# Kernel optimization log

Measured on AMD Instinct MI355X. Metric: run time of the kernel, lower is better.

## Reference

```python
import jax, jax.numpy as jnp
import numpy as np

B, S, Hd = 4, 2048, 1024
NH, D = 16, 64

def setup_inputs() -> dict:
    key = jax.random.key(0)
    ks = jax.random.split(key, 8)
    scale = 0.02
    return {
        "hidden_states": jax.random.normal(ks[0], (B, S, Hd), dtype=jnp.float32),
        "attention_mask": jnp.zeros((B, 1, 1, S), dtype=jnp.float32),
        "relations": jax.random.normal(ks[1], (1, 1, S, D), dtype=jnp.float32),
        "Wq": jax.random.normal(ks[2], (Hd, Hd), dtype=jnp.float32) * scale,
        "bq": jnp.zeros((Hd,), dtype=jnp.float32),
        "Wk": jax.random.normal(ks[3], (Hd, Hd), dtype=jnp.float32) * scale,
        "bk": jnp.zeros((Hd,), dtype=jnp.float32),
        "Wv": jax.random.normal(ks[4], (Hd, Hd), dtype=jnp.float32) * scale,
        "bv": jnp.zeros((Hd,), dtype=jnp.float32),
    }

def _heads(x):  # [B,S,Hd] -> [B,NH,S,D]
    return x.reshape(x.shape[0], x.shape[1], NH, D).transpose(0, 2, 1, 3)

def _rotate_half_interleaved(x):
    # stack([-x_odd, x_even], -1).reshape_as(x)
    return jnp.stack([-x[..., 1::2], x[..., ::2]], axis=-1).reshape(x.shape)

def reference(hidden_states, attention_mask, relations, Wq, bq, Wk, bk, Wv, bv):
    q = _heads(hidden_states @ Wq.T + bq)
    k = _heads(hidden_states @ Wk.T + bk)
    v = _heads(hidden_states @ Wv.T + bv)

    # interleaved rotary: cos from odd slots, sin from even slots, each repeated x2
    cos_pos = jnp.repeat(relations[..., 1::2], 2, axis=-1)  # [1,1,S,D]
    sin_pos = jnp.repeat(relations[..., ::2], 2, axis=-1)
    q = q * cos_pos + _rotate_half_interleaved(q) * sin_pos
    k = k * cos_pos + _rotate_half_interleaved(k) * sin_pos

    scores = jnp.einsum("bhqd,bhkd->bhqk", q, k) / jnp.sqrt(jnp.float32(D))
    scores = scores + attention_mask
    probs = jax.nn.softmax(scores, axis=-1)
    ctx = jnp.einsum("bhqk,bhkd->bhqd", probs, v)
    return ctx.transpose(0, 2, 1, 3).reshape(hidden_states.shape[0], hidden_states.shape[1], NH * D)
```

## Files before the change

### kernel.cpp

```cpp
#include <hip/hip_runtime.h>

typedef __attribute__((ext_vector_type(8))) short short8;
typedef __attribute__((ext_vector_type(4))) float f32x4;
typedef __attribute__((ext_vector_type(4))) unsigned int u32x4;
typedef __attribute__((ext_vector_type(2))) unsigned int u32x2;
typedef __attribute__((ext_vector_type(4))) unsigned short u16x4;

#define NHEADS 16
#define DHEAD 64
#define SEQ 2048
#define BATCH 4
#define HD 1024
#define MTOT 8192

static __device__ __forceinline__ unsigned short f2b(float x) {
  unsigned u = __builtin_bit_cast(unsigned, x);
  u += 0x7fffu + ((u >> 16) & 1u);
  return (unsigned short)(u >> 16);
}

static __device__ __forceinline__ unsigned pk2h(float lo, float hi) {
  unsigned a = __builtin_bit_cast(unsigned, lo) + 0x8000u;
  unsigned b = __builtin_bit_cast(unsigned, hi) + 0x8000u;
  return (a >> 16) | (b & 0xffff0000u);
}

static __device__ __forceinline__ void gll16(const void* g, void* l) {
  __builtin_amdgcn_global_load_lds(
      (const __attribute__((address_space(1))) unsigned int*)g,
      (__attribute__((address_space(3))) unsigned int*)l, 16, 0, 0);
}

__global__ void cvt_bf16(const float* __restrict__ src,
                         unsigned short* __restrict__ dst, int n4) {
  int i = blockIdx.x * blockDim.x + threadIdx.x;
  if (i < n4) {
    f32x4 v = ((const f32x4*)src)[i];
    u16x4 o;
    o[0] = f2b(v[0]); o[1] = f2b(v[1]); o[2] = f2b(v[2]); o[3] = f2b(v[3]);
    ((u16x4*)dst)[i] = o;
  }
}

#define WQ4 (HD * HD / 4)
__global__ void prep(const float* __restrict__ Wq, const float* __restrict__ Wk,
                     const float* __restrict__ Wv, const float* __restrict__ mask,
                     unsigned short* __restrict__ Wb,
                     unsigned short* __restrict__ Wm) {
  int i = blockIdx.x * blockDim.x + threadIdx.x;
  if (i < 3 * WQ4) {
    int rg = i / WQ4;
    int idx = i - rg * WQ4;
    const float* src = (rg == 0) ? Wq : (rg == 1) ? Wk : Wv;
    f32x4 v = ((const f32x4*)src)[idx];
    u16x4 o;
    o[0] = f2b(v[0]); o[1] = f2b(v[1]); o[2] = f2b(v[2]); o[3] = f2b(v[3]);
    ((u16x4*)(Wb + (size_t)rg * HD * HD))[idx] = o;
  } else {
    int j = i - 3 * WQ4;
    f32x4 v = ((const f32x4*)mask)[j];
    u16x4 o;
    o[0] = f2b(__expf(v[0])); o[1] = f2b(__expf(v[1]));
    o[2] = f2b(__expf(v[2])); o[3] = f2b(__expf(v[3]));
    ((u16x4*)Wm)[j] = o;
  }
}

__global__ __launch_bounds__(256) void qkv_gemm(
    const unsigned short* __restrict__ X,
    const unsigned short* __restrict__ Wall,
    const float* __restrict__ bq, const float* __restrict__ bk,
    const float* __restrict__ bv,
    const float* __restrict__ rel,
    const float* __restrict__ mask,
    unsigned short* __restrict__ Qo,
    unsigned short* __restrict__ Ko,
    unsigned short* __restrict__ Vt) {
  __shared__ __align__(16) unsigned short As[128 * 64];
  __shared__ __align__(16) unsigned short Bs[128 * 64];

  const int t = threadIdx.x;
  const int lane = t & 63;
  const int w = t >> 6;

  const int n = blockIdx.x;
  const int xcd = n & 7;
  const int li = n >> 3;
  const int pp = xcd * 3 + (li >> 6);
  const int bx = li & 63;
  const int by = pp & 7;
  const int bz = pp >> 3;

  const unsigned short* W = Wall + (size_t)bz * HD * HD;
  const int m0 = bx * 128;
  const int n0 = by * 128;

  f32x4 acc[4][4];
  for (int i = 0; i < 4; i++)
    for (int j = 0; j < 4; j++) acc[i][j] = (f32x4){0.f, 0.f, 0.f, 0.f};

  const int wm = (w & 1) * 64;
  const int wn = (w >> 1) * 64;
  const int cl = lane & 15;
  const int qd = lane >> 4;

  for (int k0 = 0; k0 < HD; k0 += 64) {
    __syncthreads();
#pragma unroll
    for (int j = 0; j < 4; j++) {
      int r0 = w * 32 + j * 8;
      int r = r0 + (lane >> 3);
      int cg = (((lane & 7) ^ (r & 7)) << 3);
      gll16(X + (size_t)(m0 + r) * HD + k0 + cg, As + r0 * 64);
      gll16(W + (size_t)(n0 + r) * HD + k0 + cg, Bs + r0 * 64);
    }
    __syncthreads();

#pragma unroll
    for (int ks = 0; ks < 2; ks++) {
      const int cc = ks * 4 + qd;
      short8 af[4], bf[4];
#pragma unroll
      for (int i = 0; i < 4; i++) {
        int r = wm + i * 16 + cl;
        af[i] = *(const short8*)(As + r * 64 + ((cc ^ (r & 7)) << 3));
      }
#pragma unroll
      for (int j = 0; j < 4; j++) {
        int r = wn + j * 16 + cl;
        bf[j] = *(const short8*)(Bs + r * 64 + ((cc ^ (r & 7)) << 3));
      }
      if (bz < 2) {
#pragma unroll
        for (int i = 0; i < 4; i++)
#pragma unroll
          for (int j = 0; j < 4; j++)
            acc[i][j] = __builtin_amdgcn_mfma_f32_16x16x32_bf16(bf[j], af[i],
                                                                acc[i][j], 0, 0, 0);
      } else {
#pragma unroll
        for (int i = 0; i < 4; i++)
#pragma unroll
          for (int j = 0; j < 4; j++)
            acc[i][j] = __builtin_amdgcn_mfma_f32_16x16x32_bf16(af[i], bf[j],
                                                                acc[i][j], 0, 0, 0);
      }
    }
  }

  if (bz == 2) {
    const int hh = (n0 + wn) >> 6;
#pragma unroll
    for (int i = 0; i < 4; i++) {
      int mb = m0 + wm + i * 16 + qd * 4;
      int bb = mb >> 11, ssb = mb & (SEQ - 1);
      f32x4 mk = *(const f32x4*)(mask + bb * SEQ + ssb);
      f32x4 w4;
#pragma unroll
      for (int r = 0; r < 4; r++) w4[r] = __expf(mk[r]);
      int colp = (ssb & ~31) | ((ssb & 12) << 1) | (((ssb >> 4) & 1) << 2);
#pragma unroll
      for (int j = 0; j < 4; j++) {
        int nn = n0 + wn + j * 16 + cl;
        int dd = j * 16 + cl;
        float bn = bv[nn];
        u32x2 pk;
        pk[0] = pk2h((acc[i][j][0] + bn) * w4[0], (acc[i][j][1] + bn) * w4[1]);
        pk[1] = pk2h((acc[i][j][2] + bn) * w4[2], (acc[i][j][3] + bn) * w4[3]);
        *(u32x2*)(Vt + ((size_t)((bb * NHEADS + hh) * DHEAD + dd)) * SEQ + colp) = pk;
      }
    }
  } else {
    const float* bias = (bz == 0) ? bq : bk;
    unsigned short* Out = (bz == 0) ? Qo : Ko;
    const float qs = (bz == 0) ? 0.125f * 1.4426950408889634f : 1.0f;
    const int hh = (n0 + wn) >> 6;
#pragma unroll
    for (int j = 0; j < 4; j++) {
      int nb = n0 + wn + j * 16 + qd * 4;
      f32x4 b4 = *(const f32x4*)(bias + nb);
      int ddb = j * 16 + qd * 4;
#pragma unroll
      for (int i = 0; i < 4; i++) {
        int s = m0 + wm + i * 16 + cl;
        int bb = s >> 11, ss = s & (SEQ - 1);
        f32x4 rl = *(const f32x4*)(rel + ss * DHEAD + ddb);
        float x0 = acc[i][j][0] + b4[0];
        float x1 = acc[i][j][1] + b4[1];
        float x2 = acc[i][j][2] + b4[2];
        float x3 = acc[i][j][3] + b4[3];
        float y0 = (x0 * rl[1] - x1 * rl[0]) * qs;
        float y1 = (x1 * rl[1] + x0 * rl[0]) * qs;
        float y2 = (x2 * rl[3] - x3 * rl[2]) * qs;
        float y3 = (x3 * rl[3] + x2 * rl[2]) * qs;
        u32x2 pk;
        pk[0] = pk2h(y0, y1);
        pk[1] = pk2h(y2, y3);
        *(u32x2*)(Out + (((size_t)(bb * NHEADS + hh)) * SEQ + ss) * DHEAD + ddb) = pk;
      }
    }
  }
}

__global__ __launch_bounds__(256, 2) void attn(
    const unsigned short* __restrict__ Q,
    const unsigned short* __restrict__ K,
    const unsigned short* __restrict__ Vt,
    const unsigned short* __restrict__ wmask,
    float* __restrict__ out) {
  __shared__ __align__(16) unsigned short Ks[2][128 * 64];
  __shared__ __align__(16) unsigned short Vs[2][64 * 128];

  const int t = threadIdx.x;
  const int lane = t & 63;
  const int w = t >> 6;

  const int n = blockIdx.x;
  const int xcd = n & 7;
  const int li = n >> 3;
  const int bh = xcd * 8 + (li >> 4);
  const int qt = li & 15;

  const int b = bh >> 4, h = bh & 15;
  const int s0 = qt * 128;
  const unsigned short* Qp = Q + (size_t)bh * SEQ * DHEAD;
  const unsigned short* Kp = K + (size_t)bh * SEQ * DHEAD;
  const unsigned short* Vp = Vt + (size_t)bh * DHEAD * SEQ;
  const unsigned short* wmp = wmask + b * SEQ;

  const int cl = lane & 15;
  const int qd = lane >> 4;

  short8 qf[2][2];
#pragma unroll
  for (int mt = 0; mt < 2; mt++)
#pragma unroll
    for (int ks = 0; ks < 2; ks++)
      qf[mt][ks] = *(const short8*)(Qp + (size_t)(s0 + w * 32 + mt * 16 + cl) * DHEAD +
                                    ks * 32 + qd * 8);

  f32x4 ov[2][4];
  f32x4 ovl[2];
#pragma unroll
  for (int mt = 0; mt < 2; mt++) {
    ovl[mt] = (f32x4){0.f, 0.f, 0.f, 0.f};
#pragma unroll
    for (int dt = 0; dt < 4; dt++) ov[mt][dt] = (f32x4){0.f, 0.f, 0.f, 0.f};
  }

  auto stage = [&](int bi, int kt) {
#pragma unroll
    for (int j = 0; j < 4; j++) {
      int r0 = w * 32 + j * 8;
      int r = r0 + (lane >> 3);
      int c = (lane & 7) ^ (r & 7);
      gll16(Kp + (size_t)(kt + r) * DHEAD + c * 8, &Ks[bi][r0 * 64]);
    }
#pragma unroll
    for (int j = 0; j < 4; j++) {
      int r0 = w * 16 + j * 4;
      int r = r0 + (lane >> 4);
      int c = (lane & 15) ^ (r & 7);
      gll16(Vp + (size_t)r * SEQ + kt + c * 8, &Vs[bi][r0 * 128]);
    }
  };

  stage(0, 0);

  for (int it = 0; it < SEQ / 128; it++) {
    const int kt = it * 128;
    const int bi = it & 1;
    __syncthreads();
    if (it + 1 < SEQ / 128) stage(1 - bi, kt + 128);
    const unsigned short* Ksb = &Ks[bi][0];
    const unsigned short* Vsb = &Vs[bi][0];

    short8 wf[4];
#pragma unroll
    for (int c = 0; c < 4; c++) {
      u32x2 w0 = *(const u32x2*)(wmp + kt + c * 32 + qd * 4);
      u32x2 w1 = *(const u32x2*)(wmp + kt + c * 32 + 16 + qd * 4);
      u32x4 ww = {w0[0], w0[1], w1[0], w1[1]};
      wf[c] = __builtin_bit_cast(short8, ww);
    }

    f32x4 sc[2][8];
#pragma unroll
    for (int mt = 0; mt < 2; mt++)
#pragma unroll
      for (int nt = 0; nt < 8; nt++) sc[mt][nt] = (f32x4){0.f, 0.f, 0.f, 0.f};
#pragma unroll
    for (int ks = 0; ks < 2; ks++) {
#pragma unroll
      for (int nt = 0; nt < 8; nt++) {
        int krow = nt * 16 + cl;
        short8 kf = *(const short8*)(Ksb + krow * 64 +
                                     (((ks * 4 + qd) ^ (krow & 7)) << 3));
        sc[0][nt] = __builtin_amdgcn_mfma_f32_16x16x32_bf16(kf, qf[0][ks], sc[0][nt], 0, 0, 0);
        sc[1][nt] = __builtin_amdgcn_mfma_f32_16x16x32_bf16(kf, qf[1][ks], sc[1][nt], 0, 0, 0);
      }
    }

    unsigned pw[2][8][2];
#pragma unroll
    for (int mt = 0; mt < 2; mt++) {
#pragma unroll
      for (int nt = 0; nt < 8; nt++) {
        float p0 = __builtin_amdgcn_exp2f(sc[mt][nt][0]);
        float p1 = __builtin_amdgcn_exp2f(sc[mt][nt][1]);
        float p2 = __builtin_amdgcn_exp2f(sc[mt][nt][2]);
        float p3 = __builtin_amdgcn_exp2f(sc[mt][nt][3]);
        pw[mt][nt][0] = pk2h(p0, p1);
        pw[mt][nt][1] = pk2h(p2, p3);
      }
    }

#pragma unroll
    for (int c = 0; c < 4; c++) {
      u32x4 bb0 = {pw[0][2 * c][0], pw[0][2 * c][1], pw[0][2 * c + 1][0], pw[0][2 * c + 1][1]};
      u32x4 bb1 = {pw[1][2 * c][0], pw[1][2 * c][1], pw[1][2 * c + 1][0], pw[1][2 * c + 1][1]};
      short8 bf0 = __builtin_bit_cast(short8, bb0);
      short8 bf1 = __builtin_bit_cast(short8, bb1);
      ovl[0] = __builtin_amdgcn_mfma_f32_16x16x32_bf16(wf[c], bf0, ovl[0], 0, 0, 0);
      ovl[1] = __builtin_amdgcn_mfma_f32_16x16x32_bf16(wf[c], bf1, ovl[1], 0, 0, 0);
#pragma unroll
      for (int dt = 0; dt < 4; dt++) {
        int vrow = dt * 16 + cl;
        short8 vf = *(const short8*)(Vsb + vrow * 128 +
                                     (((c * 4 + qd) ^ (vrow & 7)) << 3));
        ov[0][dt] = __builtin_amdgcn_mfma_f32_16x16x32_bf16(vf, bf0, ov[0][dt], 0, 0, 0);
        ov[1][dt] = __builtin_amdgcn_mfma_f32_16x16x32_bf16(vf, bf1, ov[1][dt], 0, 0, 0);
      }
    }
  }

#pragma unroll
  for (int mt = 0; mt < 2; mt++) {
    float rl = 1.0f / ovl[mt][0];
    int s = s0 + w * 32 + mt * 16 + cl;
    float* ob = out + ((size_t)b * SEQ + s) * HD + h * DHEAD;
#pragma unroll
    for (int dt = 0; dt < 4; dt++) {
      f32x4 o;
      o[0] = ov[mt][dt][0] * rl;
      o[1] = ov[mt][dt][1] * rl;
      o[2] = ov[mt][dt][2] * rl;
      o[3] = ov[mt][dt][3] * rl;
      *(f32x4*)(ob + dt * 16 + qd * 4) = o;
    }
  }
}

extern "C" void kernel_launch(void* const* d_in, const int* in_sizes, int n_in,
                              void* d_out, int out_size, void* d_ws, size_t ws_size,
                              hipStream_t stream) {
  const float* hidden = (const float*)d_in[0];
  const float* mask   = (const float*)d_in[1];
  const float* rel    = (const float*)d_in[2];
  const float* Wq     = (const float*)d_in[3];
  const float* bq     = (const float*)d_in[4];
  const float* Wk     = (const float*)d_in[5];
  const float* bk     = (const float*)d_in[6];
  const float* Wv     = (const float*)d_in[7];
  const float* bv     = (const float*)d_in[8];
  float* out = (float*)d_out;

  unsigned short* Xb = (unsigned short*)d_ws;
  unsigned short* Wb = Xb + (size_t)MTOT * HD;
  unsigned short* Qb = Wb + (size_t)3 * HD * HD;
  unsigned short* Kb = Qb + (size_t)MTOT * HD;
  unsigned short* Vb = Kb + (size_t)MTOT * HD;
  unsigned short* Wm = Vb + (size_t)MTOT * HD;

  {
    int n4 = MTOT * HD / 4;
    cvt_bf16<<<n4 / 256, 256, 0, stream>>>(hidden, Xb, n4);
  }
  prep<<<(3 * WQ4 + BATCH * SEQ / 4) / 256, 256, 0, stream>>>(Wq, Wk, Wv, mask, Wb, Wm);
  qkv_gemm<<<dim3(1536), 256, 0, stream>>>(Xb, Wb, bq, bk, bv, rel, mask, Qb, Kb, Vb);
  attn<<<dim3(1024), 256, 0, stream>>>(Qb, Kb, Vb, Wm, out);
}
```

Measured before the change: 306.6 us.

## Rewrite QKV GEMM as 256x256 tiles with 8 waves and double-buffered LDS pipeline

The QKV projection GEMM moves from 128x128 tiles with 4 waves and a single LDS buffer to 256x256 tiles with 8 waves, double-buffered LDS, and a phased schedule. Within each phase, sub-tile global-to-LDS loads for future k-steps are interleaved with MFMA work, using explicit barriers, waitcnt and setprio. This is meant to hide global load latency and raise data reuse per tile. The cost is more registers and LDS per block (64KB), and only 384 blocks, which may underfill the GPU's compute units.

```diff
diff --git a/kernel.cpp b/kernel.cpp
--- a/kernel.cpp
+++ b/kernel.cpp
@@ -66,7 +66,7 @@
   }
 }
 
-__global__ __launch_bounds__(256) void qkv_gemm(
+__global__ __launch_bounds__(512) void qkv_gemm(
     const unsigned short* __restrict__ X,
     const unsigned short* __restrict__ Wall,
     const float* __restrict__ bq, const float* __restrict__ bk,
@@ -76,83 +76,150 @@
     unsigned short* __restrict__ Qo,
     unsigned short* __restrict__ Ko,
     unsigned short* __restrict__ Vt) {
-  __shared__ __align__(16) unsigned short As[128 * 64];
-  __shared__ __align__(16) unsigned short Bs[128 * 64];
+  __shared__ __align__(16) unsigned short As[2][256 * 64];
+  __shared__ __align__(16) unsigned short Bs[2][256 * 64];
 
   const int t = threadIdx.x;
   const int lane = t & 63;
   const int w = t >> 6;
+  const int wm = w >> 2;
+  const int wn = w & 3;
 
   const int n = blockIdx.x;
   const int xcd = n & 7;
   const int li = n >> 3;
-  const int pp = xcd * 3 + (li >> 6);
-  const int bx = li & 63;
-  const int by = pp & 7;
-  const int bz = pp >> 3;
-
-  const unsigned short* W = Wall + (size_t)bz * HD * HD;
-  const int m0 = bx * 128;
-  const int n0 = by * 128;
-
-  f32x4 acc[4][4];
-  for (int i = 0; i < 4; i++)
-    for (int j = 0; j < 4; j++) acc[i][j] = (f32x4){0.f, 0.f, 0.f, 0.f};
-
-  const int wm = (w & 1) * 64;
-  const int wn = (w >> 1) * 64;
+  const int bx = xcd * 4 + (li & 3);
+  const int pp = li >> 2;
+  const int by = pp & 3;
+  const int bz = pp >> 2;
+
+  const unsigned short* Wp = Wall + (size_t)bz * HD * HD;
+  const int m0 = bx * 256;
+  const int n0 = by * 256;
+
   const int cl = lane & 15;
   const int qd = lane >> 4;
-
-  for (int k0 = 0; k0 < HD; k0 += 64) {
-    __syncthreads();
-#pragma unroll
-    for (int j = 0; j < 4; j++) {
-      int r0 = w * 32 + j * 8;
-      int r = r0 + (lane >> 3);
-      int cg = (((lane & 7) ^ (r & 7)) << 3);
-      gll16(X + (size_t)(m0 + r) * HD + k0 + cg, As + r0 * 64);
-      gll16(W + (size_t)(n0 + r) * HD + k0 + cg, Bs + r0 * 64);
-    }
-    __syncthreads();
-
-#pragma unroll
-    for (int ks = 0; ks < 2; ks++) {
-      const int cc = ks * 4 + qd;
-      short8 af[4], bf[4];
-#pragma unroll
-      for (int i = 0; i < 4; i++) {
-        int r = wm + i * 16 + cl;
-        af[i] = *(const short8*)(As + r * 64 + ((cc ^ (r & 7)) << 3));
-      }
-#pragma unroll
-      for (int j = 0; j < 4; j++) {
-        int r = wn + j * 16 + cl;
-        bf[j] = *(const short8*)(Bs + r * 64 + ((cc ^ (r & 7)) << 3));
-      }
-      if (bz < 2) {
-#pragma unroll
-        for (int i = 0; i < 4; i++)
-#pragma unroll
-          for (int j = 0; j < 4; j++)
-            acc[i][j] = __builtin_amdgcn_mfma_f32_16x16x32_bf16(bf[j], af[i],
-                                                                acc[i][j], 0, 0, 0);
-      } else {
-#pragma unroll
-        for (int i = 0; i < 4; i++)
-#pragma unroll
-          for (int j = 0; j < 4; j++)
-            acc[i][j] = __builtin_amdgcn_mfma_f32_16x16x32_bf16(af[i], bf[j],
-                                                                acc[i][j], 0, 0, 0);
-      }
-    }
+  const int lr = lane >> 3;
+  const int cgl = (((lane & 7) ^ (lane >> 3)) << 3);
+
+  f32x4 acc[8][4];
+#pragma unroll
+  for (int i = 0; i < 8; i++)
+#pragma unroll
+    for (int j = 0; j < 4; j++) acc[i][j] = (f32x4){0.f, 0.f, 0.f, 0.f};
+
+  auto stageA = [&](int b, int q, int k0) {
+#pragma unroll
+    for (int u = 0; u < 2; u++) {
+      int v = w * 2 + u;
+      int ar = ((v >> 3) << 7) + (q << 6) + ((v & 7) << 3);
+      gll16(X + (size_t)(m0 + ar + lr) * HD + k0 + cgl, &As[b][ar * 64]);
+    }
+  };
+  auto stageB = [&](int b, int q, int k0) {
+#pragma unroll
+    for (int u = 0; u < 2; u++) {
+      int v = w * 2 + u;
+      int br = ((v >> 2) << 6) + (q << 5) + ((v & 3) << 3);
+      gll16(Wp + (size_t)(n0 + br + lr) * HD + k0 + cgl, &Bs[b][br * 64]);
+    }
+  };
+
+  short8 af[4][2];
+
+#define PHASE(bi, qm, qn, LOADA, STG)                                          \
+  {                                                                            \
+    if (LOADA) {                                                               \
+      _Pragma("unroll") for (int i = 0; i < 4; i++) {                          \
+        int r = wm * 128 + (qm) * 64 + i * 16 + cl;                            \
+        const unsigned short* rp = &As[bi][r * 64];                            \
+        _Pragma("unroll") for (int ks = 0; ks < 2; ks++)                       \
+          af[i][ks] = *(const short8*)(rp + (((ks * 4 + qd) ^ (r & 7)) << 3)); \
+      }                                                                        \
+    }                                                                          \
+    short8 bf[2][2];                                                           \
+    _Pragma("unroll") for (int j = 0; j < 2; j++) {                            \
+      int r = wn * 64 + (qn) * 32 + j * 16 + cl;                               \
+      const unsigned short* rp = &Bs[bi][r * 64];                              \
+      _Pragma("unroll") for (int ks = 0; ks < 2; ks++)                         \
+        bf[j][ks] = *(const short8*)(rp + (((ks * 4 + qd) ^ (r & 7)) << 3));   \
+    }                                                                          \
+    STG;                                                                       \
+    __builtin_amdgcn_s_barrier();                                              \
+    asm volatile("s_waitcnt lgkmcnt(0)");                                      \
+    __builtin_amdgcn_sched_barrier(0);                                         \
+    __builtin_amdgcn_s_setprio(1);                                             \
+    if (bz < 2) {                                                              \
+      _Pragma("unroll") for (int i = 0; i < 4; i++)                            \
+        _Pragma("unroll") for (int j = 0; j < 2; j++)                          \
+          _Pragma("unroll") for (int ks = 0; ks < 2; ks++)                     \
+            acc[(qm) * 4 + i][(qn) * 2 + j] =                                  \
+                __builtin_amdgcn_mfma_f32_16x16x32_bf16(                       \
+                    bf[j][ks], af[i][ks], acc[(qm) * 4 + i][(qn) * 2 + j],     \
+                    0, 0, 0);                                                  \
+    } else {                                                                   \
+      _Pragma("unroll") for (int i = 0; i < 4; i++)                            \
+        _Pragma("unroll") for (int j = 0; j < 2; j++)                          \
+          _Pragma("unroll") for (int ks = 0; ks < 2; ks++)                     \
+            acc[(qm) * 4 + i][(qn) * 2 + j] =                                  \
+                __builtin_amdgcn_mfma_f32_16x16x32_bf16(                       \
+                    af[i][ks], bf[j][ks], acc[(qm) * 4 + i][(qn) * 2 + j],     \
+                    0, 0, 0);                                                  \
+    }                                                                          \
+    __builtin_amdgcn_s_setprio(0);                                             \
+  }
+
+#define PH_END()                    \
+  __builtin_amdgcn_s_barrier();     \
+  __builtin_amdgcn_sched_barrier(0);
+
+#define PH_VMC()                       \
+  __builtin_amdgcn_sched_barrier(0);   \
+  asm volatile("s_waitcnt vmcnt(4)");  \
+  __builtin_amdgcn_sched_barrier(0);
+
+  stageA(0, 0, 0);
+  stageB(0, 0, 0);
+  stageA(0, 1, 0);
+  stageB(0, 1, 0);
+  stageA(1, 0, 64);
+  stageB(1, 0, 64);
+  asm volatile("s_waitcnt vmcnt(4)");
+  __builtin_amdgcn_s_barrier();
+  __builtin_amdgcn_sched_barrier(0);
+
+#pragma unroll 1
+  for (int it = 0; it < 8; it++) {
+    const int t0k = it * 128;
+    const int kB = t0k + 64;
+    const int kA = (t0k + 128) & 1023;
+    const int kC = (t0k + 192) & 1023;
+
+    PHASE(0, 0, 0, true,  stageA(1, 1, kB));
+    PH_END();
+    PHASE(0, 0, 1, false, stageB(1, 1, kB));
+    PH_END();
+    PHASE(0, 1, 0, true,  stageA(0, 0, kA));
+    PH_END();
+    PHASE(0, 1, 1, false, stageB(0, 0, kA));
+    PH_VMC();
+    PH_END();
+    PHASE(1, 0, 0, true,  stageA(0, 1, kA));
+    PH_END();
+    PHASE(1, 0, 1, false, stageB(0, 1, kA));
+    PH_END();
+    PHASE(1, 1, 0, true,  stageA(1, 0, kC));
+    PH_END();
+    PHASE(1, 1, 1, false, stageB(1, 0, kC));
+    PH_VMC();
+    PH_END();
   }
 
   if (bz == 2) {
-    const int hh = (n0 + wn) >> 6;
-#pragma unroll
-    for (int i = 0; i < 4; i++) {
-      int mb = m0 + wm + i * 16 + qd * 4;
+    const int hh = (n0 >> 6) + wn;
+#pragma unroll
+    for (int mf = 0; mf < 8; mf++) {
+      int mb = m0 + wm * 128 + mf * 16 + qd * 4;
       int bb = mb >> 11, ssb = mb & (SEQ - 1);
       f32x4 mk = *(const f32x4*)(mask + bb * SEQ + ssb);
       f32x4 w4;
@@ -160,13 +227,13 @@
       for (int r = 0; r < 4; r++) w4[r] = __expf(mk[r]);
       int colp = (ssb & ~31) | ((ssb & 12) << 1) | (((ssb >> 4) & 1) << 2);
 #pragma unroll
-      for (int j = 0; j < 4; j++) {
-        int nn = n0 + wn + j * 16 + cl;
-        int dd = j * 16 + cl;
-        float bn = bv[nn];
+      for (int nf = 0; nf < 4; nf++) {
+        int feat = n0 + wn * 64 + nf * 16 + cl;
+        int dd = nf * 16 + cl;
+        float bn = bv[feat];
         u32x2 pk;
-        pk[0] = pk2h((acc[i][j][0] + bn) * w4[0], (acc[i][j][1] + bn) * w4[1]);
-        pk[1] = pk2h((acc[i][j][2] + bn) * w4[2], (acc[i][j][3] + bn) * w4[3]);
+        pk[0] = pk2h((acc[mf][nf][0] + bn) * w4[0], (acc[mf][nf][1] + bn) * w4[1]);
+        pk[1] = pk2h((acc[mf][nf][2] + bn) * w4[2], (acc[mf][nf][3] + bn) * w4[3]);
         *(u32x2*)(Vt + ((size_t)((bb * NHEADS + hh) * DHEAD + dd)) * SEQ + colp) = pk;
       }
     }
@@ -174,21 +241,21 @@
     const float* bias = (bz == 0) ? bq : bk;
     unsigned short* Out = (bz == 0) ? Qo : Ko;
     const float qs = (bz == 0) ? 0.125f * 1.4426950408889634f : 1.0f;
-    const int hh = (n0 + wn) >> 6;
-#pragma unroll
-    for (int j = 0; j < 4; j++) {
-      int nb = n0 + wn + j * 16 + qd * 4;
+    const int hh = (n0 >> 6) + wn;
+#pragma unroll
+    for (int nf = 0; nf < 4; nf++) {
+      int nb = n0 + wn * 64 + nf * 16 + qd * 4;
       f32x4 b4 = *(const f32x4*)(bias + nb);
-      int ddb = j * 16 + qd * 4;
-#pragma unroll
-      for (int i = 0; i < 4; i++) {
-        int s = m0 + wm + i * 16 + cl;
+      int ddb = nf * 16 + qd * 4;
+#pragma unroll
+      for (int mf = 0; mf < 8; mf++) {
+        int s = m0 + wm * 128 + mf * 16 + cl;
         int bb = s >> 11, ss = s & (SEQ - 1);
         f32x4 rl = *(const f32x4*)(rel + ss * DHEAD + ddb);
-        float x0 = acc[i][j][0] + b4[0];
-        float x1 = acc[i][j][1] + b4[1];
-        float x2 = acc[i][j][2] + b4[2];
-        float x3 = acc[i][j][3] + b4[3];
+        float x0 = acc[mf][nf][0] + b4[0];
+        float x1 = acc[mf][nf][1] + b4[1];
+        float x2 = acc[mf][nf][2] + b4[2];
+        float x3 = acc[mf][nf][3] + b4[3];
         float y0 = (x0 * rl[1] - x1 * rl[0]) * qs;
         float y1 = (x1 * rl[1] + x0 * rl[0]) * qs;
         float y2 = (x2 * rl[3] - x3 * rl[2]) * qs;
@@ -200,6 +267,9 @@
       }
     }
   }
+#undef PHASE
+#undef PH_END
+#undef PH_VMC
 }
 
 __global__ __launch_bounds__(256, 2) void attn(
@@ -377,6 +447,6 @@
     cvt_bf16<<<n4 / 256, 256, 0, stream>>>(hidden, Xb, n4);
   }
   prep<<<(3 * WQ4 + BATCH * SEQ / 4) / 256, 256, 0, stream>>>(Wq, Wk, Wv, mask, Wb, Wm);
-  qkv_gemm<<<dim3(1536), 256, 0, stream>>>(Xb, Wb, bq, bk, bv, rel, mask, Qb, Kb, Vb);
+  qkv_gemm<<<dim3(384), 512, 0, stream>>>(Xb, Wb, bq, bk, bv, rel, mask, Qb, Kb, Vb);
   attn<<<dim3(1024), 256, 0, stream>>>(Qb, Kb, Vb, Wm, out);
 }
```

Result: slower. 334.9 us (+9.2%).
